# Optimization experiments

Measured on AMD Instinct MI355X. Metric: run time of the kernel, lower is better.

The kernel has to match this reference:

```python
import jax, jax.numpy as jnp
import numpy as np

N_NODES = 50000
N_EDGES = 800000
N_GRAPHS = 128
IN_C, HID_C, OUT_C = 128, 256, 128


def setup_inputs() -> dict:
    key = jax.random.key(0)
    ks = jax.random.split(key, 10)
    x = jax.random.normal(ks[0], (N_NODES, IN_C), dtype=jnp.float32)
    edge_index = jax.random.randint(ks[1], (2, N_EDGES), 0, N_NODES, dtype=jnp.int32)
    batch = jnp.sort(jax.random.randint(ks[2], (N_NODES,), 0, N_GRAPHS, dtype=jnp.int32))
    def glorot(k, fan_in, fan_out):
        lim = (6.0 / (fan_in + fan_out)) ** 0.5
        return jax.random.uniform(k, (fan_in, fan_out), jnp.float32, -lim, lim)
    W1 = glorot(ks[3], IN_C, HID_C)
    b1 = jnp.zeros((HID_C,), jnp.float32)
    W2 = glorot(ks[4], HID_C, HID_C)
    b2 = jnp.zeros((HID_C,), jnp.float32)
    Wfc = glorot(ks[5], HID_C, OUT_C)
    bfc = jnp.zeros((OUT_C,), jnp.float32)
    return {"x": x, "edge_index": edge_index, "batch": batch,
            "W1": W1, "b1": b1, "W2": W2, "b2": b2, "Wfc": Wfc, "bfc": bfc}


def _gcn_conv(x, src, dst, W, b, n_nodes):
    # PyG GCNConv: h = x @ W; out[dst] += norm * h[src]; out += b
    h = x @ W  # [N, F_out]
    ones = jnp.ones(src.shape, dtype=h.dtype)
    deg = jax.ops.segment_sum(ones, dst, num_segments=n_nodes)  # in-degree incl self loops
    dinv = jnp.where(deg > 0, jax.lax.rsqrt(deg), 0.0)
    norm = dinv[src] * dinv[dst]                    # [E]
    msg = h[src] * norm[:, None]                    # gather + scale, [E, F_out]
    out = jax.ops.segment_sum(msg, dst, num_segments=n_nodes)  # scatter-add
    return out + b


def reference(x, edge_index, batch, W1, b1, W2, b2, Wfc, bfc):
    n = x.shape[0]
    loops = jnp.arange(n, dtype=edge_index.dtype)
    src = jnp.concatenate([edge_index[0], loops])   # add self loops (GCNConv default)
    dst = jnp.concatenate([edge_index[1], loops])
    h = jax.nn.relu(_gcn_conv(x, src, dst, W1, b1, n))
    h = jax.nn.relu(_gcn_conv(h, src, dst, W2, b2, n))
    # global_mean_pool keyed by batch index
    sums = jax.ops.segment_sum(h, batch, num_segments=N_GRAPHS)          # [G, HID]
    cnts = jax.ops.segment_sum(jnp.ones((n,), h.dtype), batch, num_segments=N_GRAPHS)
    pooled = sums / jnp.maximum(cnts, 1.0)[:, None]
    return pooled @ Wfc + bfc
```

## Files before the change

### kernel.cpp

```cpp
#include <hip/hip_runtime.h>
#include <type_traits>

#define HID 256
#define INC 128
#define OUTC 128

typedef __attribute__((ext_vector_type(8))) short short8;
typedef __attribute__((ext_vector_type(4))) float floatx4;

__device__ __forceinline__ unsigned short f2bf(float f) {
    unsigned int u = __float_as_uint(f);
    unsigned int r = (u + 0x7FFFu + ((u >> 16) & 1u)) >> 16;
    return (unsigned short)r;
}

__device__ __forceinline__ void bfacc2(float* a, uint u, float nr) {
    a[0] = fmaf(nr, __uint_as_float(u << 16), a[0]);
    a[1] = fmaf(nr, __uint_as_float(u & 0xFFFF0000u), a[1]);
}

__global__ void k_convX(const float* __restrict__ x, unsigned short* __restrict__ xb, int total4) {
    int i = blockIdx.x * 256 + threadIdx.x;
    if (i < total4) {
        const float4 v = *(const float4*)(x + (size_t)i * 4);
        uint2 o;
        o.x = (unsigned)f2bf(v.x) | ((unsigned)f2bf(v.y) << 16);
        o.y = (unsigned)f2bf(v.z) | ((unsigned)f2bf(v.w) << 16);
        *(uint2*)(xb + (size_t)i * 4) = o;
    }
}

__global__ void k_hist(const int* __restrict__ dst, int* __restrict__ cnt, int e) {
    int i = blockIdx.x * blockDim.x + threadIdx.x;
    if (i < e) atomicAdd(&cnt[dst[i]], 1);
}

__global__ __launch_bounds__(256) void k_scan_local(const int* __restrict__ cnt,
                                                    int* __restrict__ ex, int* __restrict__ blk_sum,
                                                    float* __restrict__ dinv, int n) {
    __shared__ int s[256];
    const int t = threadIdx.x;
    const int i = blockIdx.x * 256 + t;
    const int v = (i < n) ? cnt[i] : 0;
    if (i < n) dinv[i] = rsqrtf((float)v + 1.0f);
    s[t] = v;
    __syncthreads();
    for (int off = 1; off < 256; off <<= 1) {
        int add = (t >= off) ? s[t - off] : 0;
        __syncthreads();
        s[t] += add;
        __syncthreads();
    }
    if (i < n) ex[i] = s[t] - v;
    if (t == 255) blk_sum[blockIdx.x] = s[255];
}

__global__ __launch_bounds__(256) void k_scan_blk(int* __restrict__ blk_sum, int nb) {
    __shared__ int s[256];
    const int t = threadIdx.x;
    const int v = (t < nb) ? blk_sum[t] : 0;
    s[t] = v;
    __syncthreads();
    for (int off = 1; off < 256; off <<= 1) {
        int add = (t >= off) ? s[t - off] : 0;
        __syncthreads();
        s[t] += add;
        __syncthreads();
    }
    if (t < nb) blk_sum[t] = s[t] - v;
}

__global__ void k_scan_add(int* __restrict__ row_ptr, const int* __restrict__ blk_sum,
                           int* __restrict__ cnt, int n, int e) {
    int i = blockIdx.x * 256 + threadIdx.x;
    if (i < n) { row_ptr[i] += blk_sum[i >> 8]; cnt[i] = 0; }
    if (i == 0) row_ptr[n] = e;
}

__global__ void k_fill(const int* __restrict__ src, const int* __restrict__ dst,
                       const int* __restrict__ row_ptr, int* __restrict__ cursor,
                       int* __restrict__ csr_src, int e) {
    int i = blockIdx.x * blockDim.x + threadIdx.x;
    if (i < e) {
        const int d = dst[i];
        const int pos = row_ptr[d] + atomicAdd(&cursor[d], 1);
        csr_src[pos] = src[i];
    }
}

__global__ void k_convW(const float* __restrict__ W, unsigned short* __restrict__ Wt, int K) {
    int id = blockIdx.x * 256 + threadIdx.x;
    if (id < K * HID) {
        int n = id / K;
        int k = id - n * K;
        Wt[id] = f2bf(W[k * HID + n]);
    }
}

template <int CH>
__global__ __launch_bounds__(256) void k_agg(const unsigned short* __restrict__ h,
                                             const int* __restrict__ row_ptr,
                                             const int* __restrict__ csr_src,
                                             const float* __restrict__ dinv,
                                             unsigned short* __restrict__ out, int n) {
    constexpr int CPL = CH / 64;
    using VT = std::conditional_t<CPL == 2, uint, uint2>;
    const int v = (blockIdx.x * 256 + threadIdx.x) >> 6;
    const int lane = threadIdx.x & 63;
    if (v >= n) return;
    const float dv = dinv[v];
    const unsigned short* hl = h + lane * CPL;

    float acc[CPL];
    {
        const VT u = *(const VT*)(hl + (size_t)v * CH);
        const float s2 = dv * dv;
        if constexpr (CPL == 2) {
            acc[0] = s2 * __uint_as_float(((uint)u) << 16);
            acc[1] = s2 * __uint_as_float(((uint)u) & 0xFFFF0000u);
        } else {
            const uint2 w = (uint2)u;
            acc[0] = s2 * __uint_as_float(w.x << 16);
            acc[1] = s2 * __uint_as_float(w.x & 0xFFFF0000u);
            acc[2] = s2 * __uint_as_float(w.y << 16);
            acc[3] = s2 * __uint_as_float(w.y & 0xFFFF0000u);
        }
    }

    const int beg = row_ptr[v];
    const int end = row_ptr[v + 1];
    int i = beg;
    for (; i + 4 <= end; i += 4) {
        const int s0 = csr_src[i];
        const int s1 = csr_src[i + 1];
        const int s2i = csr_src[i + 2];
        const int s3 = csr_src[i + 3];
        const float n0 = dv * dinv[s0];
        const float n1 = dv * dinv[s1];
        const float n2 = dv * dinv[s2i];
        const float n3 = dv * dinv[s3];
        const VT r0 = *(const VT*)(hl + (size_t)s0 * CH);
        const VT r1 = *(const VT*)(hl + (size_t)s1 * CH);
        const VT r2 = *(const VT*)(hl + (size_t)s2i * CH);
        const VT r3 = *(const VT*)(hl + (size_t)s3 * CH);
        if constexpr (CPL == 2) {
            bfacc2(acc, (uint)r0, n0);
            bfacc2(acc, (uint)r1, n1);
            bfacc2(acc, (uint)r2, n2);
            bfacc2(acc, (uint)r3, n3);
        } else {
            const uint2 w0 = (uint2)r0, w1 = (uint2)r1, w2 = (uint2)r2, w3 = (uint2)r3;
            bfacc2(acc, w0.x, n0); bfacc2(acc + 2, w0.y, n0);
            bfacc2(acc, w1.x, n1); bfacc2(acc + 2, w1.y, n1);
            bfacc2(acc, w2.x, n2); bfacc2(acc + 2, w2.y, n2);
            bfacc2(acc, w3.x, n3); bfacc2(acc + 2, w3.y, n3);
        }
    }
    for (; i < end; ++i) {
        const int s0 = csr_src[i];
        const float n0 = dv * dinv[s0];
        const VT r0 = *(const VT*)(hl + (size_t)s0 * CH);
        if constexpr (CPL == 2) {
            bfacc2(acc, (uint)r0, n0);
        } else {
            const uint2 w0 = (uint2)r0;
            bfacc2(acc, w0.x, n0); bfacc2(acc + 2, w0.y, n0);
        }
    }

    if constexpr (CPL == 2) {
        uint o = (unsigned)f2bf(acc[0]) | ((unsigned)f2bf(acc[1]) << 16);
        *(uint*)(out + (size_t)v * CH + lane * CPL) = o;
    } else {
        uint2 o;
        o.x = (unsigned)f2bf(acc[0]) | ((unsigned)f2bf(acc[1]) << 16);
        o.y = (unsigned)f2bf(acc[2]) | ((unsigned)f2bf(acc[3]) << 16);
        *(uint2*)(out + (size_t)v * CH + lane * CPL) = o;
    }
}

template <int K, bool RELU, typename OT>
__global__ __launch_bounds__(256) void k_gemm_mfma(const unsigned short* __restrict__ A,
                                                   const unsigned short* __restrict__ Wt,
                                                   const float* __restrict__ bias,
                                                   OT* __restrict__ out, int M) {
    constexpr int LDA = K + 8;
    __shared__ unsigned short sA[32 * LDA];
    const int t = threadIdx.x;
    const int row0 = blockIdx.x * 32;

    {
        const int r = t >> 3;
        const int c0 = (t & 7) * (K / 8);
        unsigned short* dstp = &sA[r * LDA + c0];
        if (row0 + r < M) {
            const unsigned short* srcp = A + (size_t)(row0 + r) * K + c0;
#pragma unroll
            for (int j = 0; j < K / 8; j += 8)
                *(uint4*)(dstp + j) = *(const uint4*)(srcp + j);
        } else {
            const uint4 z = {0, 0, 0, 0};
#pragma unroll
            for (int j = 0; j < K / 8; j += 8) *(uint4*)(dstp + j) = z;
        }
    }
    __syncthreads();

    const int wv = t >> 6;
    const int lane = t & 63;
    const int m16 = lane & 15;
    const int quad = lane >> 4;

    floatx4 acc[2][4];
#pragma unroll
    for (int h2 = 0; h2 < 2; ++h2)
#pragma unroll
        for (int j = 0; j < 4; ++j) acc[h2][j] = (floatx4){0.f, 0.f, 0.f, 0.f};

    const unsigned short* ap0 = &sA[m16 * LDA + quad * 8];
    const unsigned short* ap1 = &sA[(16 + m16) * LDA + quad * 8];
    const unsigned short* bp = Wt + (size_t)(wv * 64 + m16) * K + quad * 8;

#pragma unroll
    for (int k0 = 0; k0 < K; k0 += 32) {
        const short8 a0 = *(const short8*)(ap0 + k0);
        const short8 a1 = *(const short8*)(ap1 + k0);
        const short8 b0 = *(const short8*)(bp + 0 * 16 * K + k0);
        const short8 b1 = *(const short8*)(bp + 1 * 16 * K + k0);
        const short8 b2 = *(const short8*)(bp + 2 * 16 * K + k0);
        const short8 b3 = *(const short8*)(bp + 3 * 16 * K + k0);
        acc[0][0] = __builtin_amdgcn_mfma_f32_16x16x32_bf16(a0, b0, acc[0][0], 0, 0, 0);
        acc[0][1] = __builtin_amdgcn_mfma_f32_16x16x32_bf16(a0, b1, acc[0][1], 0, 0, 0);
        acc[0][2] = __builtin_amdgcn_mfma_f32_16x16x32_bf16(a0, b2, acc[0][2], 0, 0, 0);
        acc[0][3] = __builtin_amdgcn_mfma_f32_16x16x32_bf16(a0, b3, acc[0][3], 0, 0, 0);
        acc[1][0] = __builtin_amdgcn_mfma_f32_16x16x32_bf16(a1, b0, acc[1][0], 0, 0, 0);
        acc[1][1] = __builtin_amdgcn_mfma_f32_16x16x32_bf16(a1, b1, acc[1][1], 0, 0, 0);
        acc[1][2] = __builtin_amdgcn_mfma_f32_16x16x32_bf16(a1, b2, acc[1][2], 0, 0, 0);
        acc[1][3] = __builtin_amdgcn_mfma_f32_16x16x32_bf16(a1, b3, acc[1][3], 0, 0, 0);
    }

    const int nbase = wv * 64 + m16;
    const float bb0 = bias[nbase + 0];
    const float bb1 = bias[nbase + 16];
    const float bb2 = bias[nbase + 32];
    const float bb3 = bias[nbase + 48];
#pragma unroll
    for (int h2 = 0; h2 < 2; ++h2) {
#pragma unroll
        for (int j = 0; j < 4; ++j) {
            const int row = row0 + h2 * 16 + quad * 4 + j;
            if (row >= M) continue;
            float v0 = acc[h2][0][j] + bb0;
            float v1 = acc[h2][1][j] + bb1;
            float v2 = acc[h2][2][j] + bb2;
            float v3 = acc[h2][3][j] + bb3;
            if constexpr (RELU) {
                v0 = fmaxf(v0, 0.f); v1 = fmaxf(v1, 0.f);
                v2 = fmaxf(v2, 0.f); v3 = fmaxf(v3, 0.f);
            }
            if constexpr (sizeof(OT) == 4) {
                out[(size_t)row * HID + nbase + 0]  = v0;
                out[(size_t)row * HID + nbase + 16] = v1;
                out[(size_t)row * HID + nbase + 32] = v2;
                out[(size_t)row * HID + nbase + 48] = v3;
            } else {
                out[(size_t)row * HID + nbase + 0]  = f2bf(v0);
                out[(size_t)row * HID + nbase + 16] = f2bf(v1);
                out[(size_t)row * HID + nbase + 32] = f2bf(v2);
                out[(size_t)row * HID + nbase + 48] = f2bf(v3);
            }
        }
    }
}

#define POOL_CHUNK 64
__global__ __launch_bounds__(256) void k_pool_partial(const float* __restrict__ h,
                                                      const int* __restrict__ batch,
                                                      float* __restrict__ pooled_sum, int n) {
    const int c = threadIdx.x;
    const int v0 = blockIdx.x * POOL_CHUNK;
    const int v1 = min(v0 + POOL_CHUNK, n);
    if (v0 >= n) return;
    int cur_g = batch[v0];
    float sum = 0.0f;
    for (int v = v0; v < v1; ++v) {
        const int g = batch[v];
        const float val = fmaxf(h[(size_t)v * HID + c], 0.0f);
        if (g != cur_g) {
            atomicAdd(&pooled_sum[cur_g * HID + c], sum);
            sum = 0.0f;
            cur_g = g;
        }
        sum += val;
    }
    atomicAdd(&pooled_sum[cur_g * HID + c], sum);
}

__global__ void k_fc(const float* __restrict__ pooled_sum, const int* __restrict__ batch,
                     const float* __restrict__ W, const float* __restrict__ b,
                     float* __restrict__ out, int n) {
    const int g = blockIdx.x;
    const int c = threadIdx.x;
    int a = 0, hi = n;
    while (a < hi) { int m = (a + hi) >> 1; if (batch[m] < g) a = m + 1; else hi = m; }
    const int start = a;
    hi = n;
    while (a < hi) { int m = (a + hi) >> 1; if (batch[m] < g + 1) a = m + 1; else hi = m; }
    const float cnt = (float)(a - start);

    float acc = 0.0f;
    const float* p = pooled_sum + g * HID;
    for (int k = 0; k < HID; ++k) acc += p[k] * W[k * OUTC + c];
    out[g * OUTC + c] = acc / fmaxf(cnt, 1.0f) + b[c];
}

extern "C" void kernel_launch(void* const* d_in, const int* in_sizes, int n_in,
                              void* d_out, int out_size, void* d_ws, size_t ws_size,
                              hipStream_t stream) {
    const float* x   = (const float*)d_in[0];
    const int*   ei  = (const int*)d_in[1];
    const int*   bat = (const int*)d_in[2];
    const float* W1  = (const float*)d_in[3];
    const float* b1  = (const float*)d_in[4];
    const float* W2  = (const float*)d_in[5];
    const float* b2  = (const float*)d_in[6];
    const float* Wfc = (const float*)d_in[7];
    const float* bfc = (const float*)d_in[8];
    float* out = (float*)d_out;

    const int n = in_sizes[2];
    const int e = in_sizes[1] / 2;
    const int* src = ei;
    const int* dst = ei + e;
    const int nb = (n + 255) / 256;

    size_t off = 0;
    auto alloc = [&](size_t bytes) {
        char* p = (char*)d_ws + off;
        off += (bytes + 255) & ~(size_t)255;
        return p;
    };
    int*   cnt     = (int*)alloc((size_t)n * 4);
    int*   row_ptr = (int*)alloc((size_t)(n + 1) * 4);
    int*   blk_sum = (int*)alloc(512 * 4);
    int*   csr_src = (int*)alloc((size_t)e * 4);
    float* dinv    = (float*)alloc((size_t)n * 4);
    unsigned short* Wt1 = (unsigned short*)alloc((size_t)INC * HID * 2);
    unsigned short* Wt2 = (unsigned short*)alloc((size_t)HID * HID * 2);
    unsigned short* R1  = (unsigned short*)alloc((size_t)n * HID * 2);
    unsigned short* R2  = (unsigned short*)alloc((size_t)n * INC * 2);
    unsigned short* R3  = (unsigned short*)alloc((size_t)n * HID * 2);
    float* out2   = (float*)alloc((size_t)n * HID * 4);
    float* pooled = (float*)alloc((size_t)128 * HID * 4);

    const int TB = 256;
    hipMemsetAsync(cnt, 0, (size_t)n * 4, stream);
    hipMemsetAsync(pooled, 0, (size_t)128 * HID * 4, stream);

    k_convX<<<((n * INC / 4) + TB - 1) / TB, TB, 0, stream>>>(x, R1, n * INC / 4);

    k_hist<<<(e + TB - 1) / TB, TB, 0, stream>>>(dst, cnt, e);
    k_scan_local<<<nb, TB, 0, stream>>>(cnt, row_ptr, blk_sum, dinv, n);
    k_scan_blk<<<1, TB, 0, stream>>>(blk_sum, nb);
    k_scan_add<<<nb, TB, 0, stream>>>(row_ptr, blk_sum, cnt, n, e);
    k_fill<<<(e + TB - 1) / TB, TB, 0, stream>>>(src, dst, row_ptr, cnt, csr_src, e);

    k_convW<<<INC, TB, 0, stream>>>(W1, Wt1, INC);
    k_convW<<<HID, TB, 0, stream>>>(W2, Wt2, HID);

    const int gemm_blocks = (n + 31) / 32;
    const int agg_blocks = (n + 3) / 4;

    k_agg<INC><<<agg_blocks, TB, 0, stream>>>(R1, row_ptr, csr_src, dinv, R2, n);
    k_gemm_mfma<INC, true, unsigned short><<<gemm_blocks, TB, 0, stream>>>(R2, Wt1, b1, R3, n);

    k_agg<HID><<<agg_blocks, TB, 0, stream>>>(R3, row_ptr, csr_src, dinv, R1, n);
    k_gemm_mfma<HID, false, float><<<gemm_blocks, TB, 0, stream>>>(R1, Wt2, b2, out2, n);

    k_pool_partial<<<(n + POOL_CHUNK - 1) / POOL_CHUNK, TB, 0, stream>>>(out2, bat, pooled, n);
    k_fc<<<128, 128, 0, stream>>>(pooled, bat, Wfc, bfc, out, n);
}
```

Before: 360.5 us.

## Fuse mean-pool into second GEMM epilogue, merge scan and weight-convert kernels

```diff
diff --git a/kernel.cpp b/kernel.cpp
--- a/kernel.cpp
+++ b/kernel.cpp
@@ -55,25 +55,21 @@
     if (t == 255) blk_sum[blockIdx.x] = s[255];
 }
 
-__global__ __launch_bounds__(256) void k_scan_blk(int* __restrict__ blk_sum, int nb) {
+__global__ __launch_bounds__(256) void k_scan_add(int* __restrict__ row_ptr,
+                                                  const int* __restrict__ blk_sum,
+                                                  int* __restrict__ cnt, int n, int e) {
     __shared__ int s[256];
     const int t = threadIdx.x;
-    const int v = (t < nb) ? blk_sum[t] : 0;
-    s[t] = v;
+    const int b = blockIdx.x;
+    s[t] = (t < b) ? blk_sum[t] : 0;
     __syncthreads();
-    for (int off = 1; off < 256; off <<= 1) {
-        int add = (t >= off) ? s[t - off] : 0;
+    for (int off = 128; off > 0; off >>= 1) {
+        if (t < off) s[t] += s[t + off];
         __syncthreads();
-        s[t] += add;
-        __syncthreads();
-    }
-    if (t < nb) blk_sum[t] = s[t] - v;
-}
-
-__global__ void k_scan_add(int* __restrict__ row_ptr, const int* __restrict__ blk_sum,
-                           int* __restrict__ cnt, int n, int e) {
-    int i = blockIdx.x * 256 + threadIdx.x;
-    if (i < n) { row_ptr[i] += blk_sum[i >> 8]; cnt[i] = 0; }
+    }
+    const int offset = s[0];
+    const int i = b * 256 + t;
+    if (i < n) { row_ptr[i] += offset; cnt[i] = 0; }
     if (i == 0) row_ptr[n] = e;
 }
 
@@ -88,12 +84,18 @@
     }
 }
 
-__global__ void k_convW(const float* __restrict__ W, unsigned short* __restrict__ Wt, int K) {
+__global__ void k_convW(const float* __restrict__ W1, unsigned short* __restrict__ Wt1,
+                        const float* __restrict__ W2, unsigned short* __restrict__ Wt2) {
     int id = blockIdx.x * 256 + threadIdx.x;
-    if (id < K * HID) {
-        int n = id / K;
-        int k = id - n * K;
-        Wt[id] = f2bf(W[k * HID + n]);
+    if (id < INC * HID) {
+        int n = id / INC;
+        int k = id - n * INC;
+        Wt1[id] = f2bf(W1[k * HID + n]);
+    } else if (id < INC * HID + HID * HID) {
+        int id2 = id - INC * HID;
+        int n = id2 / HID;
+        int k = id2 - n * HID;
+        Wt2[id2] = f2bf(W2[k * HID + n]);
     }
 }
 
@@ -130,30 +132,25 @@
     const int beg = row_ptr[v];
     const int end = row_ptr[v + 1];
     int i = beg;
-    for (; i + 4 <= end; i += 4) {
-        const int s0 = csr_src[i];
-        const int s1 = csr_src[i + 1];
-        const int s2i = csr_src[i + 2];
-        const int s3 = csr_src[i + 3];
-        const float n0 = dv * dinv[s0];
-        const float n1 = dv * dinv[s1];
-        const float n2 = dv * dinv[s2i];
-        const float n3 = dv * dinv[s3];
-        const VT r0 = *(const VT*)(hl + (size_t)s0 * CH);
-        const VT r1 = *(const VT*)(hl + (size_t)s1 * CH);
-        const VT r2 = *(const VT*)(hl + (size_t)s2i * CH);
-        const VT r3 = *(const VT*)(hl + (size_t)s3 * CH);
-        if constexpr (CPL == 2) {
-            bfacc2(acc, (uint)r0, n0);
-            bfacc2(acc, (uint)r1, n1);
-            bfacc2(acc, (uint)r2, n2);
-            bfacc2(acc, (uint)r3, n3);
-        } else {
-            const uint2 w0 = (uint2)r0, w1 = (uint2)r1, w2 = (uint2)r2, w3 = (uint2)r3;
-            bfacc2(acc, w0.x, n0); bfacc2(acc + 2, w0.y, n0);
-            bfacc2(acc, w1.x, n1); bfacc2(acc + 2, w1.y, n1);
-            bfacc2(acc, w2.x, n2); bfacc2(acc + 2, w2.y, n2);
-            bfacc2(acc, w3.x, n3); bfacc2(acc + 2, w3.y, n3);
+    for (; i + 8 <= end; i += 8) {
+        int si[8];
+        float nr[8];
+        VT r[8];
+#pragma unroll
+        for (int j = 0; j < 8; ++j) si[j] = csr_src[i + j];
+#pragma unroll
+        for (int j = 0; j < 8; ++j) nr[j] = dv * dinv[si[j]];
+#pragma unroll
+        for (int j = 0; j < 8; ++j) r[j] = *(const VT*)(hl + (size_t)si[j] * CH);
+#pragma unroll
+        for (int j = 0; j < 8; ++j) {
+            if constexpr (CPL == 2) {
+                bfacc2(acc, (uint)r[j], nr[j]);
+            } else {
+                const uint2 w = (uint2)r[j];
+                bfacc2(acc, w.x, nr[j]);
+                bfacc2(acc + 2, w.y, nr[j]);
+            }
         }
     }
     for (; i < end; ++i) {
@@ -179,13 +176,16 @@
     }
 }
 
-template <int K, bool RELU, typename OT>
+template <int K, bool RELU, bool POOL, typename OT>
 __global__ __launch_bounds__(256) void k_gemm_mfma(const unsigned short* __restrict__ A,
                                                    const unsigned short* __restrict__ Wt,
                                                    const float* __restrict__ bias,
-                                                   OT* __restrict__ out, int M) {
+                                                   OT* __restrict__ out,
+                                                   const int* __restrict__ batch,
+                                                   float* __restrict__ pooled_sum, int M) {
     constexpr int LDA = K + 8;
     __shared__ unsigned short sA[32 * LDA];
+    __shared__ int s_batch[32];
     const int t = threadIdx.x;
     const int row0 = blockIdx.x * 32;
 
@@ -202,6 +202,9 @@
             const uint4 z = {0, 0, 0, 0};
 #pragma unroll
             for (int j = 0; j < K / 8; j += 8) *(uint4*)(dstp + j) = z;
+        }
+        if constexpr (POOL) {
+            if (t < 32) s_batch[t] = (row0 + t < M) ? batch[row0 + t] : -1;
         }
     }
     __syncthreads();
@@ -244,56 +247,70 @@
     const float bb1 = bias[nbase + 16];
     const float bb2 = bias[nbase + 32];
     const float bb3 = bias[nbase + 48];
-#pragma unroll
-    for (int h2 = 0; h2 < 2; ++h2) {
-#pragma unroll
-        for (int j = 0; j < 4; ++j) {
-            const int row = row0 + h2 * 16 + quad * 4 + j;
-            if (row >= M) continue;
-            float v0 = acc[h2][0][j] + bb0;
-            float v1 = acc[h2][1][j] + bb1;
-            float v2 = acc[h2][2][j] + bb2;
-            float v3 = acc[h2][3][j] + bb3;
-            if constexpr (RELU) {
-                v0 = fmaxf(v0, 0.f); v1 = fmaxf(v1, 0.f);
-                v2 = fmaxf(v2, 0.f); v3 = fmaxf(v3, 0.f);
+
+    if constexpr (POOL) {
+        float ps0 = 0.f, ps1 = 0.f, ps2 = 0.f, ps3 = 0.f;
+        int gcur = -1;
+#pragma unroll
+        for (int h2 = 0; h2 < 2; ++h2) {
+#pragma unroll
+            for (int j = 0; j < 4; ++j) {
+                const int rl = h2 * 16 + quad * 4 + j;
+                const int g = s_batch[rl];
+                if (g < 0) continue;
+                if (g != gcur) {
+                    if (gcur >= 0) {
+                        float* pp = pooled_sum + gcur * HID + nbase;
+                        atomicAdd(pp + 0, ps0);
+                        atomicAdd(pp + 16, ps1);
+                        atomicAdd(pp + 32, ps2);
+                        atomicAdd(pp + 48, ps3);
+                    }
+                    ps0 = ps1 = ps2 = ps3 = 0.f;
+                    gcur = g;
+                }
+                ps0 += fmaxf(acc[h2][0][j] + bb0, 0.f);
+                ps1 += fmaxf(acc[h2][1][j] + bb1, 0.f);
+                ps2 += fmaxf(acc[h2][2][j] + bb2, 0.f);
+                ps3 += fmaxf(acc[h2][3][j] + bb3, 0.f);
             }
-            if constexpr (sizeof(OT) == 4) {
-                out[(size_t)row * HID + nbase + 0]  = v0;
-                out[(size_t)row * HID + nbase + 16] = v1;
-                out[(size_t)row * HID + nbase + 32] = v2;
-                out[(size_t)row * HID + nbase + 48] = v3;
-            } else {
-                out[(size_t)row * HID + nbase + 0]  = f2bf(v0);
-                out[(size_t)row * HID + nbase + 16] = f2bf(v1);
-                out[(size_t)row * HID + nbase + 32] = f2bf(v2);
-                out[(size_t)row * HID + nbase + 48] = f2bf(v3);
+        }
+        if (gcur >= 0) {
+            float* pp = pooled_sum + gcur * HID + nbase;
+            atomicAdd(pp + 0, ps0);
+            atomicAdd(pp + 16, ps1);
+            atomicAdd(pp + 32, ps2);
+            atomicAdd(pp + 48, ps3);
+        }
+    } else {
+#pragma unroll
+        for (int h2 = 0; h2 < 2; ++h2) {
+#pragma unroll
+            for (int j = 0; j < 4; ++j) {
+                const int row = row0 + h2 * 16 + quad * 4 + j;
+                if (row >= M) continue;
+                float v0 = acc[h2][0][j] + bb0;
+                float v1 = acc[h2][1][j] + bb1;
+                float v2 = acc[h2][2][j] + bb2;
+                float v3 = acc[h2][3][j] + bb3;
+                if constexpr (RELU) {
+                    v0 = fmaxf(v0, 0.f); v1 = fmaxf(v1, 0.f);
+                    v2 = fmaxf(v2, 0.f); v3 = fmaxf(v3, 0.f);
+                }
+                if constexpr (sizeof(OT) == 4) {
+                    out[(size_t)row * HID + nbase + 0]  = v0;
+                    out[(size_t)row * HID + nbase + 16] = v1;
+                    out[(size_t)row * HID + nbase + 32] = v2;
+                    out[(size_t)row * HID + nbase + 48] = v3;
+                } else {
+                    out[(size_t)row * HID + nbase + 0]  = f2bf(v0);
+                    out[(size_t)row * HID + nbase + 16] = f2bf(v1);
+                    out[(size_t)row * HID + nbase + 32] = f2bf(v2);
+                    out[(size_t)row * HID + nbase + 48] = f2bf(v3);
+                }
             }
         }
     }
-}
-
-#define POOL_CHUNK 64
-__global__ __launch_bounds__(256) void k_pool_partial(const float* __restrict__ h,
-                                                      const int* __restrict__ batch,
-                                                      float* __restrict__ pooled_sum, int n) {
-    const int c = threadIdx.x;
-    const int v0 = blockIdx.x * POOL_CHUNK;
-    const int v1 = min(v0 + POOL_CHUNK, n);
-    if (v0 >= n) return;
-    int cur_g = batch[v0];
-    float sum = 0.0f;
-    for (int v = v0; v < v1; ++v) {
-        const int g = batch[v];
-        const float val = fmaxf(h[(size_t)v * HID + c], 0.0f);
-        if (g != cur_g) {
-            atomicAdd(&pooled_sum[cur_g * HID + c], sum);
-            sum = 0.0f;
-            cur_g = g;
-        }
-        sum += val;
-    }
-    atomicAdd(&pooled_sum[cur_g * HID + c], sum);
 }
 
 __global__ void k_fc(const float* __restrict__ pooled_sum, const int* __restrict__ batch,
@@ -350,7 +367,6 @@
     unsigned short* R1  = (unsigned short*)alloc((size_t)n * HID * 2);
     unsigned short* R2  = (unsigned short*)alloc((size_t)n * INC * 2);
     unsigned short* R3  = (unsigned short*)alloc((size_t)n * HID * 2);
-    float* out2   = (float*)alloc((size_t)n * HID * 4);
     float* pooled = (float*)alloc((size_t)128 * HID * 4);
 
     const int TB = 256;
@@ -361,22 +377,21 @@
 
     k_hist<<<(e + TB - 1) / TB, TB, 0, stream>>>(dst, cnt, e);
     k_scan_local<<<nb, TB, 0, stream>>>(cnt, row_ptr, blk_sum, dinv, n);
-    k_scan_blk<<<1, TB, 0, stream>>>(blk_sum, nb);
     k_scan_add<<<nb, TB, 0, stream>>>(row_ptr, blk_sum, cnt, n, e);
     k_fill<<<(e + TB - 1) / TB, TB, 0, stream>>>(src, dst, row_ptr, cnt, csr_src, e);
 
-    k_convW<<<INC, TB, 0, stream>>>(W1, Wt1, INC);
-    k_convW<<<HID, TB, 0, stream>>>(W2, Wt2, HID);
+    k_convW<<<(INC * HID + HID * HID + TB - 1) / TB, TB, 0, stream>>>(W1, Wt1, W2, Wt2);
 
     const int gemm_blocks = (n + 31) / 32;
     const int agg_blocks = (n + 3) / 4;
 
     k_agg<INC><<<agg_blocks, TB, 0, stream>>>(R1, row_ptr, csr_src, dinv, R2, n);
-    k_gemm_mfma<INC, true, unsigned short><<<gemm_blocks, TB, 0, stream>>>(R2, Wt1, b1, R3, n);
+    k_gemm_mfma<INC, true, false, unsigned short><<<gemm_blocks, TB, 0, stream>>>(
+        R2, Wt1, b1, R3, nullptr, nullptr, n);
 
     k_agg<HID><<<agg_blocks, TB, 0, stream>>>(R3, row_ptr, csr_src, dinv, R1, n);
-    k_gemm_mfma<HID, false, float><<<gemm_blocks, TB, 0, stream>>>(R1, Wt2, b2, out2, n);
-
-    k_pool_partial<<<(n + POOL_CHUNK - 1) / POOL_CHUNK, TB, 0, stream>>>(out2, bat, pooled, n);
+    k_gemm_mfma<HID, true, true, float><<<gemm_blocks, TB, 0, stream>>>(
+        R1, Wt2, b2, (float*)nullptr, bat, pooled, n);
+
     k_fc<<<128, 128, 0, stream>>>(pooled, bat, Wfc, bfc, out, n);
 }
```

Result: no change. 358.5 us (-0.6%).
